# Kernel tuning notes

Hardware: AMD Instinct MI355X
Metric: run time of the kernel (lower is better)

Reference implementation:

```python
import jax, jax.numpy as jnp
import numpy as np

D_MODEL = 2048
HQ = 32          # query heads
HKV = 8          # kv heads
HD = D_MODEL // HQ   # head_dim = 64
G = HQ // HKV        # group size = 4
THETA = 10000.0


def _rope(x, pos):
    """x: (B, H, T, D), pos: (B, T) int. Rotates even/odd interleaved pairs."""
    D = x.shape[-1]
    inv_freq = THETA ** (-jnp.arange(0, D, 2, dtype=jnp.float32) / D)   # (D/2,)
    ang = pos[:, None, :, None].astype(jnp.float32) * inv_freq          # (B,1,T,D/2)
    cos, sin = jnp.cos(ang), jnp.sin(ang)
    x1, x2 = x[..., 0::2], x[..., 1::2]
    r1 = x1 * cos - x2 * sin
    r2 = x1 * sin + x2 * cos
    return jnp.stack([r1, r2], axis=-1).reshape(x.shape)


def setup_inputs() -> dict:
    key = jax.random.key(0)
    ks = jax.random.split(key, 5)
    B, T = 2, 2048
    s = lambda fan_in: 1.0 / np.sqrt(fan_in)
    return {
        "x": jax.random.normal(ks[0], (B, T, D_MODEL), jnp.float32),
        "token_positions": jnp.arange(T, dtype=jnp.int32),
        "WQ": jax.random.normal(ks[1], (HQ * HD, D_MODEL), jnp.float32) * s(D_MODEL),
        "WK": jax.random.normal(ks[2], (HKV * HD, D_MODEL), jnp.float32) * s(D_MODEL),
        "WV": jax.random.normal(ks[3], (HKV * HD, D_MODEL), jnp.float32) * s(D_MODEL),
        "WO": jax.random.normal(ks[4], (D_MODEL, HQ * HD), jnp.float32) * s(HQ * HD),
    }


def reference(x, token_positions, WQ, WK, WV, WO):
    B, T, _ = x.shape
    pos = token_positions if token_positions.ndim == 2 else jnp.broadcast_to(token_positions[None, :], (B, T))

    # Projections (Linear is y = x @ W.T, no bias)
    Q = (x @ WQ.T).reshape(B, T, HQ, HD).transpose(0, 2, 1, 3)    # (B,Hq,T,D)
    K = (x @ WK.T).reshape(B, T, HKV, HD).transpose(0, 2, 1, 3)   # (B,Hkv,T,D)
    V = (x @ WV.T).reshape(B, T, HKV, HD).transpose(0, 2, 1, 3)

    Q = _rope(Q, pos)
    K = _rope(K, pos)

    # GQA: group query heads per kv head instead of duplicating K/V
    Qg = Q.reshape(B, HKV, G, T, HD)
    scale = jnp.float32(1.0 / np.sqrt(HD))
    scores = jnp.einsum('bkgqd,bkld->bkgql', Qg, K) * scale       # (B,Hkv,G,T,T)

    causal = jnp.tril(jnp.ones((T, T), dtype=bool))
    scores = jnp.where(causal, scores, jnp.finfo(scores.dtype).min)
    A = jax.nn.softmax(scores, axis=-1)

    O = jnp.einsum('bkgql,bkld->bkgqd', A, V)                     # (B,Hkv,G,T,D)
    O = O.reshape(B, HQ, T, HD).transpose(0, 2, 1, 3).reshape(B, T, HQ * HD)
    return O @ WO.T
```

## Files before the change

kernel.cpp:

```cpp
#include <hip/hip_runtime.h>
#include <hip/hip_bf16.h>

#define B_   2
#define T_   2048
#define DM_  2048
#define HQ_  32
#define HKV_ 8
#define HD_  64

typedef __attribute__((ext_vector_type(8))) short bf16x8;
typedef __attribute__((ext_vector_type(4))) float f32x4;
typedef __fp16 f16x4 __attribute__((ext_vector_type(4)));
typedef __fp16 f16x2 __attribute__((ext_vector_type(2)));

__device__ __forceinline__ unsigned short f2bf(float f) {
    unsigned int u = __float_as_uint(f);
    u = (u + 0x7fffu + ((u >> 16) & 1u)) >> 16;
    return (unsigned short)u;
}

__device__ __forceinline__ void gload16(const unsigned short* g, unsigned short* l) {
    __builtin_amdgcn_global_load_lds(
        (const __attribute__((address_space(1))) unsigned int*)g,
        (__attribute__((address_space(3))) unsigned int*)l, 16, 0, 0);
}


#define CONV_N 4718592

__global__ __launch_bounds__(256) void convert_all(
    const float* __restrict__ x,  const float* __restrict__ WQ,
    const float* __restrict__ WK, const float* __restrict__ WV,
    const float* __restrict__ WO, unsigned short* __restrict__ ws,
    const int* __restrict__ pos,  float* __restrict__ trig)
{
    int i = blockIdx.x*256 + threadIdx.x;
    if (i >= CONV_N) {
        int j = i - CONV_N;
        if (j < T_*32) {
            int t = j >> 5, p = j & 31;
            float inv = exp2f(-0.4152410118609203f * (float)p);
            float ang = (float)pos[t] * inv;
            float sn, cs;
            sincosf(ang, &sn, &cs);
            *(float2*)&trig[j*2] = make_float2(cs, sn);
        }
        return;
    }
    const float* src; unsigned short* dst; int rel;
    if (i < 2097152)      { src = x;  dst = ws;                 rel = i; }
    else if (i < 3145728) { src = WQ; dst = ws + 8388608;       rel = i - 2097152; }
    else if (i < 3407872) { src = WK; dst = ws + 8388608+4194304; rel = i - 3145728; }
    else if (i < 3670016) { src = WV; dst = ws + 8388608+5242880; rel = i - 3407872; }
    else                  { src = WO; dst = ws + 14680064;      rel = i - 3670016; }
    float4 v = *(const float4*)(src + (size_t)rel*4);
    uint2 pk;
    pk.x = (unsigned int)f2bf(v.x) | ((unsigned int)f2bf(v.y) << 16);
    pk.y = (unsigned int)f2bf(v.z) | ((unsigned int)f2bf(v.w) << 16);
    *(uint2*)(dst + (size_t)rel*4) = pk;
}

__global__ __launch_bounds__(256) void qkv_gemm_bf16(
    const unsigned short* __restrict__ Ab, const unsigned short* __restrict__ Wb,
    unsigned short* __restrict__ Qb, unsigned short* __restrict__ Kb,
    unsigned short* __restrict__ Vt, const float* __restrict__ trig)
{
    __shared__ unsigned short As[3][128*32];
    __shared__ unsigned short Bs[3][128*32];
    const int tid  = threadIdx.x;
    const int ln   = tid & 63;
    const int wv   = tid >> 6;
    const int wm   = (wv >> 1) * 64;
    const int wn   = (wv & 1) * 64;
    const int col  = ln & 15;
    const int quad = ln >> 4;

    const int bid = blockIdx.x;
    const int swz = (bid & 7) * 96 + (bid >> 3);
    const int n0  = (swz % 24) * 128;
    const int m0  = (swz / 24) * 128;

    const int cg = ((tid & 3) ^ ((tid >> 3) & 3)) * 8;
    const unsigned short* aG = Ab + (size_t)(m0 + (tid>>2))*DM_ + cg;
    const unsigned short* bG = Wb + (size_t)(n0 + (tid>>2))*DM_ + cg;
    const int ck = (quad ^ ((col >> 1) & 3)) * 8;

    f32x4 acc[4][4];
    #pragma unroll
    for (int i=0;i<4;++i)
        #pragma unroll
        for (int j=0;j<4;++j) { acc[i][j][0]=0.f; acc[i][j][1]=0.f; acc[i][j][2]=0.f; acc[i][j][3]=0.f; }

    auto stage = [&](int buf, int k0) {
        unsigned short* aL = &As[buf][wv*512];
        unsigned short* bL = &Bs[buf][wv*512];
        gload16(aG + k0,                  aL);
        gload16(aG + (size_t)64*DM_ + k0, aL + 2048);
        gload16(bG + k0,                  bL);
        gload16(bG + (size_t)64*DM_ + k0, bL + 2048);
    };

    auto kstep = [&](int bc, int k0v, int bstage, bool dostage, bool last) {
        if (last) asm volatile("s_waitcnt vmcnt(0)" ::: "memory");
        else      asm volatile("s_waitcnt vmcnt(4)" ::: "memory");
        __builtin_amdgcn_s_barrier();
        if (dostage) stage(bstage, k0v + 64);
        const unsigned short* Ac = As[bc];
        const unsigned short* Bc = Bs[bc];
        bf16x8 af[4], bfr[4];
        #pragma unroll
        for (int i2=0;i2<4;++i2) {
            af[i2]  = *(const bf16x8*)&Ac[(wm + i2*16 + col)*32 + ck];
            bfr[i2] = *(const bf16x8*)&Bc[(wn + i2*16 + col)*32 + ck];
        }
        #pragma unroll
        for (int i2=0;i2<4;++i2)
            #pragma unroll
            for (int j2=0;j2<4;++j2)
                acc[i2][j2] = __builtin_amdgcn_mfma_f32_16x16x32_bf16(af[i2], bfr[j2], acc[i2][j2], 0, 0, 0);
    };

    stage(0, 0);
    stage(1, 32);

    int k0 = 0;
    for (int rep = 0; rep < 20; ++rep) {
        kstep(0, k0,      2, true, false);
        kstep(1, k0+32,   0, true, false);
        kstep(2, k0+64,   1, true, false);
        k0 += 96;
    }
    kstep(0, 1920, 2, true,  false);
    kstep(1, 1952, 0, true,  false);
    kstep(2, 1984, 1, false, false);
    kstep(0, 2016, 0, false, true);

    const int b  = m0 >> 11;
    const int tb = m0 & 2047;
    #pragma unroll
    for (int j=0;j<4;++j) {
        const int n = n0 + wn + j*16 + col;
        if (n < 2560) {
            const int d   = n & 63;
            const int p   = d >> 1;
            const bool ev = (d & 1) == 0;
            const float sc = (n < 2048) ? 0.18033688011112042f : 1.0f;
            unsigned short* outp = (n < 2048)
                ? Qb + (((size_t)(b*HQ_  + (n>>6)))*T_)*HD_
                : Kb + (((size_t)(b*HKV_ + ((n-2048)>>6)))*T_)*HD_;
            #pragma unroll
            for (int i=0;i<4;++i) {
                const int t0 = tb + wm + i*16 + quad*4;
                #pragma unroll
                for (int r=0;r<4;++r) {
                    float self = acc[i][j][r];
                    float part = __shfl_xor(self, 1);
                    float2 cs  = *(const float2*)&trig[((t0 + r)*32 + p)*2];
                    float out  = ev ? (self*cs.x - part*cs.y)
                                    : (part*cs.y + self*cs.x);
                    out *= sc;
                    unsigned int pk = (unsigned int)f2bf(out);
                    unsigned int po = __shfl_xor(pk, 1);
                    if (ev)
                        *(unsigned int*)(outp + (size_t)(t0 + r)*HD_ + d) = pk | (po << 16);
                }
            }
        } else {
            #pragma unroll
            for (int i=0;i<4;++i) {
                const int t = tb + wm + i*16 + quad*4;
                unsigned short* vp = Vt + (((size_t)(b*HKV_ + ((n-2560)>>6)))*HD_ + (n&63))*T_ + t;
                union { f16x2 h; unsigned int u; } c0, c1;
                c0.h = __builtin_amdgcn_cvt_pkrtz(acc[i][j][0], acc[i][j][1]);
                c1.h = __builtin_amdgcn_cvt_pkrtz(acc[i][j][2], acc[i][j][3]);
                *(unsigned int*)(vp)     = c0.u;
                *(unsigned int*)(vp + 2) = c1.u;
            }
        }
    }
}

__global__ __launch_bounds__(256, 2) void attn_mfma(
    const unsigned short* __restrict__ Qb, const unsigned short* __restrict__ Kb,
    const unsigned short* __restrict__ Vh, unsigned short* __restrict__ Ob)
{
    __shared__ unsigned short Ks[2][64*64];
    __shared__ unsigned short Vs[2][64*64];

    const int tid  = threadIdx.x;
    const int lane = tid & 63;
    const int wave = tid >> 6;
    const int q16  = lane & 15;
    const int quad = lane >> 4;
    const int bxi  = blockIdx.x;
    const int bh   = blockIdx.y;
    const int b    = bh >> 5;
    const int h    = bh & 31;
    const int kvh  = h >> 2;
    const int qa   = bxi;
    const int qbt  = 31 - bxi;
    const int qgA  = qa *64 + wave*16 + q16;
    const int qgB  = qbt*64 + wave*16 + q16;

    const unsigned short* kbase = Kb + ((size_t)(b*HKV_ + kvh))*T_*HD_;
    const unsigned short* vbase = Vh + ((size_t)(b*HKV_ + kvh))*(size_t)HD_*T_;

    const bf16x8 qA0 = *(const bf16x8*)(Qb + ((size_t)bh*T_ + qgA)*HD_ + quad*8);
    const bf16x8 qA1 = *(const bf16x8*)(Qb + ((size_t)bh*T_ + qgA)*HD_ + 32 + quad*8);
    const bf16x8 qB0 = *(const bf16x8*)(Qb + ((size_t)bh*T_ + qgB)*HD_ + quad*8);
    const bf16x8 qB1 = *(const bf16x8*)(Qb + ((size_t)bh*T_ + qgB)*HD_ + 32 + quad*8);

    f32x4 oA[4], oB[4];
    #pragma unroll
    for (int i=0;i<4;++i) {
        oA[i][0]=0.f; oA[i][1]=0.f; oA[i][2]=0.f; oA[i][3]=0.f;
        oB[i][0]=0.f; oB[i][1]=0.f; oB[i][2]=0.f; oB[i][3]=0.f;
    }
    float lA = 0.f, lB = 0.f;

    const int sr = tid >> 3;
    const int sj = tid & 7;
    const int sc = (sj ^ (sr & 7)) * 8;

    const int rk7 = q16 & 7;
    const int ck0 = (quad ^ rk7) * 8;
    const int ck1 = ((quad + 4) ^ rk7) * 8;

    auto smrow = [&](const f32x4 s, float& ps) -> f16x4 {
        float e0 = exp2f(s[0]), e1 = exp2f(s[1]);
        float e2 = exp2f(s[2]), e3 = exp2f(s[3]);
        ps += (e0+e1) + (e2+e3);
        union { f16x2 h[2]; f16x4 v; } c;
        c.h[0] = __builtin_amdgcn_cvt_pkrtz(e0, e1);
        c.h[1] = __builtin_amdgcn_cvt_pkrtz(e2, e3);
        return c.v;
    };

    auto tile_barrier = [&]() {
        asm volatile("s_waitcnt lgkmcnt(0)" ::: "memory");
        __builtin_amdgcn_s_barrier();
        __builtin_amdgcn_sched_barrier(0);
    };

    uint4 kr0, kr1, vr0, vr1;
    kr0 = *(const uint4*)(kbase + (size_t)sr*HD_ + sj*8);
    kr1 = *(const uint4*)(kbase + (size_t)(sr+32)*HD_ + sj*8);
    vr0 = *(const uint4*)(vbase + (size_t)sr*T_ + sj*8);
    vr1 = *(const uint4*)(vbase + (size_t)(sr+32)*T_ + sj*8);
    *(uint4*)&Ks[0][sr*64 + sc]      = kr0;
    *(uint4*)&Ks[0][(sr+32)*64 + sc] = kr1;
    *(uint4*)&Vs[0][sr*64 + sc]      = vr0;
    *(uint4*)&Vs[0][(sr+32)*64 + sc] = vr1;
    kr0 = *(const uint4*)(kbase + (size_t)(64+sr)*HD_ + sj*8);
    kr1 = *(const uint4*)(kbase + (size_t)(64+sr+32)*HD_ + sj*8);
    vr0 = *(const uint4*)(vbase + (size_t)sr*T_ + 64 + sj*8);
    vr1 = *(const uint4*)(vbase + (size_t)(sr+32)*T_ + 64 + sj*8);
    __syncthreads();

    int cur = 0;

    for (int kt = 0; kt <= qa; ++kt) {
        const unsigned short* KsC = Ks[cur];
        const unsigned short* VsC = Vs[cur];
        const int nxt = cur ^ 1;

        f32x4 sB[4], sA[4];
        #pragma unroll
        for (int t=0;t<4;++t) {
            sB[t][0]=0.f; sB[t][1]=0.f; sB[t][2]=0.f; sB[t][3]=0.f;
            sA[t][0]=0.f; sA[t][1]=0.f; sA[t][2]=0.f; sA[t][3]=0.f;
        }
        f16x4 pfB[4];
        float psB = 0.f, psA = 0.f;

        __builtin_amdgcn_s_setprio(1);
        #pragma unroll
        for (int t = 0; t < 4; ++t) {
            const int rk = (t*16 + q16) * 64;
            bf16x8 a0 = *(const bf16x8*)&KsC[rk + ck0];
            bf16x8 a1 = *(const bf16x8*)&KsC[rk + ck1];
            sB[t] = __builtin_amdgcn_mfma_f32_16x16x32_bf16(a0, qB0, sB[t], 0, 0, 0);
            sB[t] = __builtin_amdgcn_mfma_f32_16x16x32_bf16(a1, qB1, sB[t], 0, 0, 0);
            sA[t] = __builtin_amdgcn_mfma_f32_16x16x32_bf16(a0, qA0, sA[t], 0, 0, 0);
            sA[t] = __builtin_amdgcn_mfma_f32_16x16x32_bf16(a1, qA1, sA[t], 0, 0, 0);
            if (t > 0) pfB[t-1] = smrow(sB[t-1], psB);
        }
        *(uint4*)&Ks[nxt][sr*64 + sc]      = kr0;
        *(uint4*)&Ks[nxt][(sr+32)*64 + sc] = kr1;
        *(uint4*)&Vs[nxt][sr*64 + sc]      = vr0;
        *(uint4*)&Vs[nxt][(sr+32)*64 + sc] = vr1;
        if (kt + 1 < qbt) {
            const int kn = (kt+2)*64;
            kr0 = *(const uint4*)(kbase + (size_t)(kn+sr)*HD_ + sj*8);
            kr1 = *(const uint4*)(kbase + (size_t)(kn+sr+32)*HD_ + sj*8);
            vr0 = *(const uint4*)(vbase + (size_t)sr*T_ + kn + sj*8);
            vr1 = *(const uint4*)(vbase + (size_t)(sr+32)*T_ + kn + sj*8);
        }
        pfB[3] = smrow(sB[3], psB);
        lB += psB;

        if (kt == qa) {
            #pragma unroll
            for (int t = 0; t < 4; ++t)
                #pragma unroll
                for (int r = 0; r < 4; ++r)
                    if (kt*64 + t*16 + quad*4 + r > qgA) sA[t][r] = -1e30f;
        }

        #pragma unroll
        for (int t = 0; t < 4; ++t) {
            const int cv = ((2*t + (quad>>1)) ^ rk7) * 8 + (quad&1)*4;
            f16x4 va[4];
            #pragma unroll
            for (int dt=0;dt<4;++dt)
                va[dt] = *(const f16x4*)&VsC[(dt*16 + q16)*64 + cv];
            #pragma unroll
            for (int dt=0;dt<4;++dt)
                oB[dt] = __builtin_amdgcn_mfma_f32_16x16x16f16(va[dt], pfB[t], oB[dt], 0, 0, 0);
            f16x4 pfA = smrow(sA[t], psA);
            #pragma unroll
            for (int dt=0;dt<4;++dt)
                oA[dt] = __builtin_amdgcn_mfma_f32_16x16x16f16(va[dt], pfA, oA[dt], 0, 0, 0);
        }
        lA += psA;
        __builtin_amdgcn_s_setprio(0);
        tile_barrier();
        cur ^= 1;
    }

    for (int kt = qa+1; kt <= qbt; ++kt) {
        const unsigned short* KsC = Ks[cur];
        const unsigned short* VsC = Vs[cur];
        const int nxt = cur ^ 1;

        f32x4 sB[4];
        #pragma unroll
        for (int t=0;t<4;++t) { sB[t][0]=0.f; sB[t][1]=0.f; sB[t][2]=0.f; sB[t][3]=0.f; }

        __builtin_amdgcn_s_setprio(1);
        #pragma unroll
        for (int t = 0; t < 4; ++t) {
            const int rk = (t*16 + q16) * 64;
            bf16x8 a0 = *(const bf16x8*)&KsC[rk + ck0];
            bf16x8 a1 = *(const bf16x8*)&KsC[rk + ck1];
            sB[t] = __builtin_amdgcn_mfma_f32_16x16x32_bf16(a0, qB0, sB[t], 0, 0, 0);
            sB[t] = __builtin_amdgcn_mfma_f32_16x16x32_bf16(a1, qB1, sB[t], 0, 0, 0);
        }
        if (kt < qbt) {
            *(uint4*)&Ks[nxt][sr*64 + sc]      = kr0;
            *(uint4*)&Ks[nxt][(sr+32)*64 + sc] = kr1;
            *(uint4*)&Vs[nxt][sr*64 + sc]      = vr0;
            *(uint4*)&Vs[nxt][(sr+32)*64 + sc] = vr1;
        }
        if (kt + 1 < qbt) {
            const int kn = (kt+2)*64;
            kr0 = *(const uint4*)(kbase + (size_t)(kn+sr)*HD_ + sj*8);
            kr1 = *(const uint4*)(kbase + (size_t)(kn+sr+32)*HD_ + sj*8);
            vr0 = *(const uint4*)(vbase + (size_t)sr*T_ + kn + sj*8);
            vr1 = *(const uint4*)(vbase + (size_t)(sr+32)*T_ + kn + sj*8);
        }
        if (kt == qbt) {
            #pragma unroll
            for (int t = 0; t < 4; ++t)
                #pragma unroll
                for (int r = 0; r < 4; ++r)
                    if (kt*64 + t*16 + quad*4 + r > qgB) sB[t][r] = -1e30f;
        }

        float psB = 0.f;
        #pragma unroll
        for (int t = 0; t < 4; ++t) {
            f16x4 pfB = smrow(sB[t], psB);
            const int cv = ((2*t + (quad>>1)) ^ rk7) * 8 + (quad&1)*4;
            #pragma unroll
            for (int dt=0;dt<4;++dt) {
                f16x4 va = *(const f16x4*)&VsC[(dt*16 + q16)*64 + cv];
                oB[dt] = __builtin_amdgcn_mfma_f32_16x16x16f16(va, pfB, oB[dt], 0, 0, 0);
            }
        }
        lB += psB;
        __builtin_amdgcn_s_setprio(0);
        tile_barrier();
        cur ^= 1;
    }

    lA += __shfl_xor(lA, 16); lA += __shfl_xor(lA, 32);
    lB += __shfl_xor(lB, 16); lB += __shfl_xor(lB, 32);
    const float rlA = 1.0f / lA;
    const float rlB = 1.0f / lB;
    unsigned short* opA = Ob + ((size_t)(b*T_ + qgA))*(HQ_*HD_) + h*HD_;
    unsigned short* opB = Ob + ((size_t)(b*T_ + qgB))*(HQ_*HD_) + h*HD_;
    #pragma unroll
    for (int dt = 0; dt < 4; ++dt) {
        uint2 pa, pb;
        pa.x = (unsigned int)f2bf(oA[dt][0]*rlA) | ((unsigned int)f2bf(oA[dt][1]*rlA) << 16);
        pa.y = (unsigned int)f2bf(oA[dt][2]*rlA) | ((unsigned int)f2bf(oA[dt][3]*rlA) << 16);
        pb.x = (unsigned int)f2bf(oB[dt][0]*rlB) | ((unsigned int)f2bf(oB[dt][1]*rlB) << 16);
        pb.y = (unsigned int)f2bf(oB[dt][2]*rlB) | ((unsigned int)f2bf(oB[dt][3]*rlB) << 16);
        *(uint2*)(opA + dt*16 + quad*4) = pa;
        *(uint2*)(opB + dt*16 + quad*4) = pb;
    }
}

__global__ __launch_bounds__(256) void out_gemm_bf16(
    const unsigned short* __restrict__ Ab, const unsigned short* __restrict__ Wb,
    float* __restrict__ C)
{
    __shared__ unsigned short As[3][128*32];
    __shared__ unsigned short Bs[3][128*32];
    const int tid  = threadIdx.x;
    const int ln   = tid & 63;
    const int wv   = tid >> 6;
    const int wm   = (wv >> 1) * 64;
    const int wn   = (wv & 1) * 64;
    const int col  = ln & 15;
    const int quad = ln >> 4;

    const int bid = blockIdx.x;
    const int swz = (bid & 7) * 64 + (bid >> 3);
    const int n0  = (swz & 15) * 128;
    const int m0  = (swz >> 4) * 128;

    const int cg = ((tid & 3) ^ ((tid >> 3) & 3)) * 8;
    const unsigned short* aG = Ab + (size_t)(m0 + (tid>>2))*DM_ + cg;
    const unsigned short* bG = Wb + (size_t)(n0 + (tid>>2))*DM_ + cg;
    const int ck = (quad ^ ((col >> 1) & 3)) * 8;

    f32x4 acc[4][4];
    #pragma unroll
    for (int i=0;i<4;++i)
        #pragma unroll
        for (int j=0;j<4;++j) { acc[i][j][0]=0.f; acc[i][j][1]=0.f; acc[i][j][2]=0.f; acc[i][j][3]=0.f; }

    auto stage = [&](int buf, int k0) {
        unsigned short* aL = &As[buf][wv*512];
        unsigned short* bL = &Bs[buf][wv*512];
        gload16(aG + k0,                  aL);
        gload16(aG + (size_t)64*DM_ + k0, aL + 2048);
        gload16(bG + k0,                  bL);
        gload16(bG + (size_t)64*DM_ + k0, bL + 2048);
    };

    auto kstep = [&](int bc, int k0v, int bstage, bool dostage, bool last) {
        if (last) asm volatile("s_waitcnt vmcnt(0)" ::: "memory");
        else      asm volatile("s_waitcnt vmcnt(4)" ::: "memory");
        __builtin_amdgcn_s_barrier();
        if (dostage) stage(bstage, k0v + 64);
        const unsigned short* Ac = As[bc];
        const unsigned short* Bc = Bs[bc];
        bf16x8 af[4], bfr[4];
        #pragma unroll
        for (int i2=0;i2<4;++i2) {
            af[i2]  = *(const bf16x8*)&Ac[(wm + i2*16 + col)*32 + ck];
            bfr[i2] = *(const bf16x8*)&Bc[(wn + i2*16 + col)*32 + ck];
        }
        #pragma unroll
        for (int i2=0;i2<4;++i2)
            #pragma unroll
            for (int j2=0;j2<4;++j2)
                acc[i2][j2] = __builtin_amdgcn_mfma_f32_16x16x32_bf16(af[i2], bfr[j2], acc[i2][j2], 0, 0, 0);
    };

    stage(0, 0);
    stage(1, 32);

    int k0 = 0;
    for (int rep = 0; rep < 20; ++rep) {
        kstep(0, k0,      2, true, false);
        kstep(1, k0+32,   0, true, false);
        kstep(2, k0+64,   1, true, false);
        k0 += 96;
    }
    kstep(0, 1920, 2, true,  false);
    kstep(1, 1952, 0, true,  false);
    kstep(2, 1984, 1, false, false);
    kstep(0, 2016, 0, false, true);

    #pragma unroll
    for (int i=0;i<4;++i) {
        const int m = m0 + wm + i*16 + quad*4;
        #pragma unroll
        for (int j=0;j<4;++j) {
            const int n = n0 + wn + j*16 + col;
            #pragma unroll
            for (int r=0;r<4;++r)
                C[(size_t)(m + r)*DM_ + n] = acc[i][j][r];
        }
    }
}

extern "C" void kernel_launch(void* const* d_in, const int* in_sizes, int n_in,
                              void* d_out, int out_size, void* d_ws, size_t ws_size,
                              hipStream_t stream) {
    const float* x   = (const float*)d_in[0];
    const int*   pos = (const int*)  d_in[1];
    const float* WQ  = (const float*)d_in[2];
    const float* WK  = (const float*)d_in[3];
    const float* WV  = (const float*)d_in[4];
    const float* WO  = (const float*)d_in[5];
    float* out = (float*)d_out;

    unsigned short* xb  = (unsigned short*)d_ws;
    unsigned short* Wb  = xb  + (size_t)8388608;
    unsigned short* WOb = Wb  + (size_t)6291456;
    unsigned short* Qb  = WOb + (size_t)4194304;
    unsigned short* Kb  = Qb  + (size_t)8388608;
    unsigned short* Vt  = Kb  + (size_t)2097152;
    unsigned short* Ob  = Vt  + (size_t)2097152;
    float* trig = (float*)Ob;

    convert_all<<<18688, 256, 0, stream>>>(x, WQ, WK, WV, WO, (unsigned short*)d_ws, pos, trig);

    qkv_gemm_bf16<<<768, 256, 0, stream>>>(xb, Wb, Qb, Kb, Vt, trig);

    dim3 g3(16, B_*HQ_);
    attn_mfma<<<g3, 256, 0, stream>>>(Qb, Kb, Vt, Ob);

    out_gemm_bf16<<<512, 256, 0, stream>>>(Ob, WOb, out);
}
```

Before: 305.5 us.

## Enlarge QKV GEMM tile to 256x256 with 8 waves per block

The QKV projection GEMM moves from 128x128 tiles with 4 waves to 256x256 tiles with 8 waves (512 threads). Each wave now computes a 128x64 sub-tile, which raises arithmetic intensity per LDS fragment load and reduces global traffic per FLOP. The trade-off is only 192 blocks on a 256-CU device, so some CUs sit idle, plus larger LDS (96KB) and higher register pressure from 32 accumulators per lane.

```diff
diff --git a/kernel.cpp b/kernel.cpp
--- a/kernel.cpp
+++ b/kernel.cpp
@@ -60,44 +60,44 @@
     *(uint2*)(dst + (size_t)rel*4) = pk;
 }
 
-__global__ __launch_bounds__(256) void qkv_gemm_bf16(
+__global__ __launch_bounds__(512, 2) void qkv_gemm_bf16(
     const unsigned short* __restrict__ Ab, const unsigned short* __restrict__ Wb,
     unsigned short* __restrict__ Qb, unsigned short* __restrict__ Kb,
     unsigned short* __restrict__ Vt, const float* __restrict__ trig)
 {
-    __shared__ unsigned short As[3][128*32];
-    __shared__ unsigned short Bs[3][128*32];
+    __shared__ unsigned short As[3][256*32];
+    __shared__ unsigned short Bs[3][256*32];
     const int tid  = threadIdx.x;
-    const int ln   = tid & 63;
+    const int lane = tid & 63;
     const int wv   = tid >> 6;
-    const int wm   = (wv >> 1) * 64;
-    const int wn   = (wv & 1) * 64;
-    const int col  = ln & 15;
-    const int quad = ln >> 4;
+    const int wr   = wv >> 2;
+    const int wc   = wv & 3;
+    const int n16  = lane & 15;
+    const int quad = lane >> 4;
 
     const int bid = blockIdx.x;
-    const int swz = (bid & 7) * 96 + (bid >> 3);
-    const int n0  = (swz % 24) * 128;
-    const int m0  = (swz / 24) * 128;
+    const int swz = (bid & 7) * 24 + (bid >> 3);
+    const int n0  = (swz % 12) * 256;
+    const int m0  = (swz / 12) * 256;
 
     const int cg = ((tid & 3) ^ ((tid >> 3) & 3)) * 8;
     const unsigned short* aG = Ab + (size_t)(m0 + (tid>>2))*DM_ + cg;
     const unsigned short* bG = Wb + (size_t)(n0 + (tid>>2))*DM_ + cg;
-    const int ck = (quad ^ ((col >> 1) & 3)) * 8;
-
-    f32x4 acc[4][4];
+    const int ck = (quad ^ ((n16 >> 1) & 3)) * 8;
+
+    f32x4 acc[8][4];
     #pragma unroll
-    for (int i=0;i<4;++i)
+    for (int i=0;i<8;++i)
         #pragma unroll
         for (int j=0;j<4;++j) { acc[i][j][0]=0.f; acc[i][j][1]=0.f; acc[i][j][2]=0.f; acc[i][j][3]=0.f; }
 
-    auto stage = [&](int buf, int k0) {
+    auto stage = [&](int buf, int k0v) {
         unsigned short* aL = &As[buf][wv*512];
         unsigned short* bL = &Bs[buf][wv*512];
-        gload16(aG + k0,                  aL);
-        gload16(aG + (size_t)64*DM_ + k0, aL + 2048);
-        gload16(bG + k0,                  bL);
-        gload16(bG + (size_t)64*DM_ + k0, bL + 2048);
+        gload16(aG + k0v,                   aL);
+        gload16(aG + (size_t)128*DM_ + k0v, aL + 4096);
+        gload16(bG + k0v,                   bL);
+        gload16(bG + (size_t)128*DM_ + k0v, bL + 4096);
     };
 
     auto kstep = [&](int bc, int k0v, int bstage, bool dostage, bool last) {
@@ -107,14 +107,15 @@
         if (dostage) stage(bstage, k0v + 64);
         const unsigned short* Ac = As[bc];
         const unsigned short* Bc = Bs[bc];
-        bf16x8 af[4], bfr[4];
-        #pragma unroll
-        for (int i2=0;i2<4;++i2) {
-            af[i2]  = *(const bf16x8*)&Ac[(wm + i2*16 + col)*32 + ck];
-            bfr[i2] = *(const bf16x8*)&Bc[(wn + i2*16 + col)*32 + ck];
-        }
-        #pragma unroll
-        for (int i2=0;i2<4;++i2)
+        bf16x8 af[8], bfr[4];
+        #pragma unroll
+        for (int i2=0;i2<8;++i2)
+            af[i2]  = *(const bf16x8*)&Ac[(wr*128 + i2*16 + n16)*32 + ck];
+        #pragma unroll
+        for (int j2=0;j2<4;++j2)
+            bfr[j2] = *(const bf16x8*)&Bc[(wc*64 + j2*16 + n16)*32 + ck];
+        #pragma unroll
+        for (int i2=0;i2<8;++i2)
             #pragma unroll
             for (int j2=0;j2<4;++j2)
                 acc[i2][j2] = __builtin_amdgcn_mfma_f32_16x16x32_bf16(af[i2], bfr[j2], acc[i2][j2], 0, 0, 0);
@@ -137,25 +138,26 @@
 
     const int b  = m0 >> 11;
     const int tb = m0 & 2047;
+    const float2* trig2 = (const float2*)trig;
     #pragma unroll
-    for (int j=0;j<4;++j) {
-        const int n = n0 + wn + j*16 + col;
+    for (int nf=0; nf<4; ++nf) {
+        const int n = n0 + wc*64 + nf*16 + n16;
         if (n < 2560) {
             const int d   = n & 63;
             const int p   = d >> 1;
             const bool ev = (d & 1) == 0;
             const float sc = (n < 2048) ? 0.18033688011112042f : 1.0f;
             unsigned short* outp = (n < 2048)
-                ? Qb + (((size_t)(b*HQ_  + (n>>6)))*T_)*HD_
-                : Kb + (((size_t)(b*HKV_ + ((n-2048)>>6)))*T_)*HD_;
-            #pragma unroll
-            for (int i=0;i<4;++i) {
-                const int t0 = tb + wm + i*16 + quad*4;
+                ? Qb + ((size_t)(b*HQ_  + (n>>6)))*T_*HD_
+                : Kb + ((size_t)(b*HKV_ + ((n-2048)>>6)))*T_*HD_;
+            #pragma unroll
+            for (int mf=0; mf<8; ++mf) {
+                const int t0 = tb + wr*128 + mf*16 + quad*4;
                 #pragma unroll
                 for (int r=0;r<4;++r) {
-                    float self = acc[i][j][r];
+                    float self = acc[mf][nf][r];
                     float part = __shfl_xor(self, 1);
-                    float2 cs  = *(const float2*)&trig[((t0 + r)*32 + p)*2];
+                    float2 cs  = trig2[(t0 + r)*32 + p];
                     float out  = ev ? (self*cs.x - part*cs.y)
                                     : (part*cs.y + self*cs.x);
                     out *= sc;
@@ -166,13 +168,15 @@
                 }
             }
         } else {
-            #pragma unroll
-            for (int i=0;i<4;++i) {
-                const int t = tb + wm + i*16 + quad*4;
-                unsigned short* vp = Vt + (((size_t)(b*HKV_ + ((n-2560)>>6)))*HD_ + (n&63))*T_ + t;
+            const int d  = n & 63;
+            const int vh = (n - 2560) >> 6;
+            #pragma unroll
+            for (int mf=0; mf<8; ++mf) {
+                const int t = tb + wr*128 + mf*16 + quad*4;
+                unsigned short* vp = Vt + ((size_t)(b*HKV_ + vh)*HD_ + d)*T_ + t;
                 union { f16x2 h; unsigned int u; } c0, c1;
-                c0.h = __builtin_amdgcn_cvt_pkrtz(acc[i][j][0], acc[i][j][1]);
-                c1.h = __builtin_amdgcn_cvt_pkrtz(acc[i][j][2], acc[i][j][3]);
+                c0.h = __builtin_amdgcn_cvt_pkrtz(acc[mf][nf][0], acc[mf][nf][1]);
+                c1.h = __builtin_amdgcn_cvt_pkrtz(acc[mf][nf][2], acc[mf][nf][3]);
                 *(unsigned int*)(vp)     = c0.u;
                 *(unsigned int*)(vp + 2) = c1.u;
             }
@@ -511,7 +515,7 @@
 
     convert_all<<<18688, 256, 0, stream>>>(x, WQ, WK, WV, WO, (unsigned short*)d_ws, pos, trig);
 
-    qkv_gemm_bf16<<<768, 256, 0, stream>>>(xb, Wb, Qb, Kb, Vt, trig);
+    qkv_gemm_bf16<<<192, 512, 0, stream>>>(xb, Wb, Qb, Kb, Vt, trig);
 
     dim3 g3(16, B_*HQ_);
     attn_mfma<<<g3, 256, 0, stream>>>(Qb, Kb, Vt, Ob);
```

New measurement: 321.1 us. 5.1% more time.

## Split paired query tiles across separate waves in 512-thread attention blocks

Applied to the files above, without the earlier changes.

The attention kernel now launches 512 threads per block. Waves 0-3 handle the long (late) query tile and waves 4-7 handle the short (early) tile, where before each wave processed both tiles. Each wave holds one set of Q, O and score registers, which lowers register pressure and lets more waves be resident. The cost is that the short-tile waves sit idle at barriers while the long tile finishes, since every wave still walks the full K/V loop to help with shared-memory loads.

```diff
diff --git a/kernel.cpp b/kernel.cpp
--- a/kernel.cpp
+++ b/kernel.cpp
@@ -180,7 +180,7 @@
     }
 }
 
-__global__ __launch_bounds__(256, 2) void attn_mfma(
+__global__ __launch_bounds__(512, 4) void attn_mfma(
     const unsigned short* __restrict__ Qb, const unsigned short* __restrict__ Kb,
     const unsigned short* __restrict__ Vh, unsigned short* __restrict__ Ob)
 {
@@ -189,7 +189,7 @@
 
     const int tid  = threadIdx.x;
     const int lane = tid & 63;
-    const int wave = tid >> 6;
+    const int wv   = tid >> 6;
     const int q16  = lane & 15;
     const int quad = lane >> 4;
     const int bxi  = blockIdx.x;
@@ -199,24 +199,20 @@
     const int kvh  = h >> 2;
     const int qa   = bxi;
     const int qbt  = 31 - bxi;
-    const int qgA  = qa *64 + wave*16 + q16;
-    const int qgB  = qbt*64 + wave*16 + q16;
+    const bool isB = (wv < 4);
+    const int  kact = isB ? qbt : qa;
+    const int  myq  = (isB ? qbt*64 + wv*16 : qa*64 + (wv-4)*16) + q16;
 
     const unsigned short* kbase = Kb + ((size_t)(b*HKV_ + kvh))*T_*HD_;
     const unsigned short* vbase = Vh + ((size_t)(b*HKV_ + kvh))*(size_t)HD_*T_;
 
-    const bf16x8 qA0 = *(const bf16x8*)(Qb + ((size_t)bh*T_ + qgA)*HD_ + quad*8);
-    const bf16x8 qA1 = *(const bf16x8*)(Qb + ((size_t)bh*T_ + qgA)*HD_ + 32 + quad*8);
-    const bf16x8 qB0 = *(const bf16x8*)(Qb + ((size_t)bh*T_ + qgB)*HD_ + quad*8);
-    const bf16x8 qB1 = *(const bf16x8*)(Qb + ((size_t)bh*T_ + qgB)*HD_ + 32 + quad*8);
-
-    f32x4 oA[4], oB[4];
-    #pragma unroll
-    for (int i=0;i<4;++i) {
-        oA[i][0]=0.f; oA[i][1]=0.f; oA[i][2]=0.f; oA[i][3]=0.f;
-        oB[i][0]=0.f; oB[i][1]=0.f; oB[i][2]=0.f; oB[i][3]=0.f;
-    }
-    float lA = 0.f, lB = 0.f;
+    const bf16x8 q0 = *(const bf16x8*)(Qb + ((size_t)bh*T_ + myq)*HD_ + quad*8);
+    const bf16x8 q1 = *(const bf16x8*)(Qb + ((size_t)bh*T_ + myq)*HD_ + 32 + quad*8);
+
+    f32x4 o[4];
+    #pragma unroll
+    for (int i=0;i<4;++i) { o[i][0]=0.f; o[i][1]=0.f; o[i][2]=0.f; o[i][3]=0.f; }
+    float l = 0.f;
 
     const int sr = tid >> 3;
     const int sj = tid & 7;
@@ -230,9 +226,9 @@
         float e0 = exp2f(s[0]), e1 = exp2f(s[1]);
         float e2 = exp2f(s[2]), e3 = exp2f(s[3]);
         ps += (e0+e1) + (e2+e3);
-        union { f16x2 h[2]; f16x4 v; } c;
-        c.h[0] = __builtin_amdgcn_cvt_pkrtz(e0, e1);
-        c.h[1] = __builtin_amdgcn_cvt_pkrtz(e2, e3);
+        union { f16x2 hh[2]; f16x4 v; } c;
+        c.hh[0] = __builtin_amdgcn_cvt_pkrtz(e0, e1);
+        c.hh[1] = __builtin_amdgcn_cvt_pkrtz(e2, e3);
         return c.v;
     };
 
@@ -242,163 +238,79 @@
         __builtin_amdgcn_sched_barrier(0);
     };
 
-    uint4 kr0, kr1, vr0, vr1;
-    kr0 = *(const uint4*)(kbase + (size_t)sr*HD_ + sj*8);
-    kr1 = *(const uint4*)(kbase + (size_t)(sr+32)*HD_ + sj*8);
-    vr0 = *(const uint4*)(vbase + (size_t)sr*T_ + sj*8);
-    vr1 = *(const uint4*)(vbase + (size_t)(sr+32)*T_ + sj*8);
-    *(uint4*)&Ks[0][sr*64 + sc]      = kr0;
-    *(uint4*)&Ks[0][(sr+32)*64 + sc] = kr1;
-    *(uint4*)&Vs[0][sr*64 + sc]      = vr0;
-    *(uint4*)&Vs[0][(sr+32)*64 + sc] = vr1;
-    kr0 = *(const uint4*)(kbase + (size_t)(64+sr)*HD_ + sj*8);
-    kr1 = *(const uint4*)(kbase + (size_t)(64+sr+32)*HD_ + sj*8);
-    vr0 = *(const uint4*)(vbase + (size_t)sr*T_ + 64 + sj*8);
-    vr1 = *(const uint4*)(vbase + (size_t)(sr+32)*T_ + 64 + sj*8);
+    uint4 kr, vr;
+    kr = *(const uint4*)(kbase + (size_t)sr*HD_ + sj*8);
+    vr = *(const uint4*)(vbase + (size_t)sr*T_ + sj*8);
+    *(uint4*)&Ks[0][sr*64 + sc] = kr;
+    *(uint4*)&Vs[0][sr*64 + sc] = vr;
+    kr = *(const uint4*)(kbase + (size_t)(64+sr)*HD_ + sj*8);
+    vr = *(const uint4*)(vbase + (size_t)sr*T_ + 64 + sj*8);
     __syncthreads();
 
     int cur = 0;
-
-    for (int kt = 0; kt <= qa; ++kt) {
-        const unsigned short* KsC = Ks[cur];
-        const unsigned short* VsC = Vs[cur];
+    for (int kt = 0; kt <= qbt; ++kt) {
         const int nxt = cur ^ 1;
-
-        f32x4 sB[4], sA[4];
-        #pragma unroll
-        for (int t=0;t<4;++t) {
-            sB[t][0]=0.f; sB[t][1]=0.f; sB[t][2]=0.f; sB[t][3]=0.f;
-            sA[t][0]=0.f; sA[t][1]=0.f; sA[t][2]=0.f; sA[t][3]=0.f;
-        }
-        f16x4 pfB[4];
-        float psB = 0.f, psA = 0.f;
-
-        __builtin_amdgcn_s_setprio(1);
-        #pragma unroll
-        for (int t = 0; t < 4; ++t) {
-            const int rk = (t*16 + q16) * 64;
-            bf16x8 a0 = *(const bf16x8*)&KsC[rk + ck0];
-            bf16x8 a1 = *(const bf16x8*)&KsC[rk + ck1];
-            sB[t] = __builtin_amdgcn_mfma_f32_16x16x32_bf16(a0, qB0, sB[t], 0, 0, 0);
-            sB[t] = __builtin_amdgcn_mfma_f32_16x16x32_bf16(a1, qB1, sB[t], 0, 0, 0);
-            sA[t] = __builtin_amdgcn_mfma_f32_16x16x32_bf16(a0, qA0, sA[t], 0, 0, 0);
-            sA[t] = __builtin_amdgcn_mfma_f32_16x16x32_bf16(a1, qA1, sA[t], 0, 0, 0);
-            if (t > 0) pfB[t-1] = smrow(sB[t-1], psB);
-        }
-        *(uint4*)&Ks[nxt][sr*64 + sc]      = kr0;
-        *(uint4*)&Ks[nxt][(sr+32)*64 + sc] = kr1;
-        *(uint4*)&Vs[nxt][sr*64 + sc]      = vr0;
-        *(uint4*)&Vs[nxt][(sr+32)*64 + sc] = vr1;
+        if (kt <= kact) {
+            const unsigned short* KsC = Ks[cur];
+            const unsigned short* VsC = Vs[cur];
+            f32x4 s[4];
+            #pragma unroll
+            for (int t=0;t<4;++t) { s[t][0]=0.f; s[t][1]=0.f; s[t][2]=0.f; s[t][3]=0.f; }
+
+            __builtin_amdgcn_s_setprio(1);
+            #pragma unroll
+            for (int t = 0; t < 4; ++t) {
+                const int rk = (t*16 + q16) * 64;
+                bf16x8 a0 = *(const bf16x8*)&KsC[rk + ck0];
+                bf16x8 a1 = *(const bf16x8*)&KsC[rk + ck1];
+                s[t] = __builtin_amdgcn_mfma_f32_16x16x32_bf16(a0, q0, s[t], 0, 0, 0);
+                s[t] = __builtin_amdgcn_mfma_f32_16x16x32_bf16(a1, q1, s[t], 0, 0, 0);
+            }
+            if (kt == kact) {
+                #pragma unroll
+                for (int t = 0; t < 4; ++t)
+                    #pragma unroll
+                    for (int r = 0; r < 4; ++r)
+                        if (kt*64 + t*16 + quad*4 + r > myq) s[t][r] = -1e30f;
+            }
+            f16x4 pf[4];
+            float ps = 0.f;
+            #pragma unroll
+            for (int t = 0; t < 4; ++t) pf[t] = smrow(s[t], ps);
+            #pragma unroll
+            for (int t = 0; t < 4; ++t) {
+                const int cv = ((2*t + (quad>>1)) ^ rk7) * 8 + (quad&1)*4;
+                #pragma unroll
+                for (int dt=0;dt<4;++dt) {
+                    f16x4 va = *(const f16x4*)&VsC[(dt*16 + q16)*64 + cv];
+                    o[dt] = __builtin_amdgcn_mfma_f32_16x16x16f16(va, pf[t], o[dt], 0, 0, 0);
+                }
+            }
+            __builtin_amdgcn_s_setprio(0);
+            l += ps;
+        }
+        if (kt < qbt) {
+            *(uint4*)&Ks[nxt][sr*64 + sc] = kr;
+            *(uint4*)&Vs[nxt][sr*64 + sc] = vr;
+        }
         if (kt + 1 < qbt) {
             const int kn = (kt+2)*64;
-            kr0 = *(const uint4*)(kbase + (size_t)(kn+sr)*HD_ + sj*8);
-            kr1 = *(const uint4*)(kbase + (size_t)(kn+sr+32)*HD_ + sj*8);
-            vr0 = *(const uint4*)(vbase + (size_t)sr*T_ + kn + sj*8);
-            vr1 = *(const uint4*)(vbase + (size_t)(sr+32)*T_ + kn + sj*8);
-        }
-        pfB[3] = smrow(sB[3], psB);
-        lB += psB;
-
-        if (kt == qa) {
-            #pragma unroll
-            for (int t = 0; t < 4; ++t)
-                #pragma unroll
-                for (int r = 0; r < 4; ++r)
-                    if (kt*64 + t*16 + quad*4 + r > qgA) sA[t][r] = -1e30f;
-        }
-
-        #pragma unroll
-        for (int t = 0; t < 4; ++t) {
-            const int cv = ((2*t + (quad>>1)) ^ rk7) * 8 + (quad&1)*4;
-            f16x4 va[4];
-            #pragma unroll
-            for (int dt=0;dt<4;++dt)
-                va[dt] = *(const f16x4*)&VsC[(dt*16 + q16)*64 + cv];
-            #pragma unroll
-            for (int dt=0;dt<4;++dt)
-                oB[dt] = __builtin_amdgcn_mfma_f32_16x16x16f16(va[dt], pfB[t], oB[dt], 0, 0, 0);
-            f16x4 pfA = smrow(sA[t], psA);
-            #pragma unroll
-            for (int dt=0;dt<4;++dt)
-                oA[dt] = __builtin_amdgcn_mfma_f32_16x16x16f16(va[dt], pfA, oA[dt], 0, 0, 0);
-        }
-        lA += psA;
-        __builtin_amdgcn_s_setprio(0);
+            kr = *(const uint4*)(kbase + (size_t)(kn+sr)*HD_ + sj*8);
+            vr = *(const uint4*)(vbase + (size_t)sr*T_ + kn + sj*8);
+        }
         tile_barrier();
         cur ^= 1;
     }
 
-    for (int kt = qa+1; kt <= qbt; ++kt) {
-        const unsigned short* KsC = Ks[cur];
-        const unsigned short* VsC = Vs[cur];
-        const int nxt = cur ^ 1;
-
-        f32x4 sB[4];
-        #pragma unroll
-        for (int t=0;t<4;++t) { sB[t][0]=0.f; sB[t][1]=0.f; sB[t][2]=0.f; sB[t][3]=0.f; }
-
-        __builtin_amdgcn_s_setprio(1);
-        #pragma unroll
-        for (int t = 0; t < 4; ++t) {
-            const int rk = (t*16 + q16) * 64;
-            bf16x8 a0 = *(const bf16x8*)&KsC[rk + ck0];
-            bf16x8 a1 = *(const bf16x8*)&KsC[rk + ck1];
-            sB[t] = __builtin_amdgcn_mfma_f32_16x16x32_bf16(a0, qB0, sB[t], 0, 0, 0);
-            sB[t] = __builtin_amdgcn_mfma_f32_16x16x32_bf16(a1, qB1, sB[t], 0, 0, 0);
-        }
-        if (kt < qbt) {
-            *(uint4*)&Ks[nxt][sr*64 + sc]      = kr0;
-            *(uint4*)&Ks[nxt][(sr+32)*64 + sc] = kr1;
-            *(uint4*)&Vs[nxt][sr*64 + sc]      = vr0;
-            *(uint4*)&Vs[nxt][(sr+32)*64 + sc] = vr1;
-        }
-        if (kt + 1 < qbt) {
-            const int kn = (kt+2)*64;
-            kr0 = *(const uint4*)(kbase + (size_t)(kn+sr)*HD_ + sj*8);
-            kr1 = *(const uint4*)(kbase + (size_t)(kn+sr+32)*HD_ + sj*8);
-            vr0 = *(const uint4*)(vbase + (size_t)sr*T_ + kn + sj*8);
-            vr1 = *(const uint4*)(vbase + (size_t)(sr+32)*T_ + kn + sj*8);
-        }
-        if (kt == qbt) {
-            #pragma unroll
-            for (int t = 0; t < 4; ++t)
-                #pragma unroll
-                for (int r = 0; r < 4; ++r)
-                    if (kt*64 + t*16 + quad*4 + r > qgB) sB[t][r] = -1e30f;
-        }
-
-        float psB = 0.f;
-        #pragma unroll
-        for (int t = 0; t < 4; ++t) {
-            f16x4 pfB = smrow(sB[t], psB);
-            const int cv = ((2*t + (quad>>1)) ^ rk7) * 8 + (quad&1)*4;
-            #pragma unroll
-            for (int dt=0;dt<4;++dt) {
-                f16x4 va = *(const f16x4*)&VsC[(dt*16 + q16)*64 + cv];
-                oB[dt] = __builtin_amdgcn_mfma_f32_16x16x16f16(va, pfB, oB[dt], 0, 0, 0);
-            }
-        }
-        lB += psB;
-        __builtin_amdgcn_s_setprio(0);
-        tile_barrier();
-        cur ^= 1;
-    }
-
-    lA += __shfl_xor(lA, 16); lA += __shfl_xor(lA, 32);
-    lB += __shfl_xor(lB, 16); lB += __shfl_xor(lB, 32);
-    const float rlA = 1.0f / lA;
-    const float rlB = 1.0f / lB;
-    unsigned short* opA = Ob + ((size_t)(b*T_ + qgA))*(HQ_*HD_) + h*HD_;
-    unsigned short* opB = Ob + ((size_t)(b*T_ + qgB))*(HQ_*HD_) + h*HD_;
+    l += __shfl_xor(l, 16); l += __shfl_xor(l, 32);
+    const float rl = 1.0f / l;
+    unsigned short* op = Ob + ((size_t)(b*T_ + myq))*(HQ_*HD_) + h*HD_;
     #pragma unroll
     for (int dt = 0; dt < 4; ++dt) {
-        uint2 pa, pb;
-        pa.x = (unsigned int)f2bf(oA[dt][0]*rlA) | ((unsigned int)f2bf(oA[dt][1]*rlA) << 16);
-        pa.y = (unsigned int)f2bf(oA[dt][2]*rlA) | ((unsigned int)f2bf(oA[dt][3]*rlA) << 16);
-        pb.x = (unsigned int)f2bf(oB[dt][0]*rlB) | ((unsigned int)f2bf(oB[dt][1]*rlB) << 16);
-        pb.y = (unsigned int)f2bf(oB[dt][2]*rlB) | ((unsigned int)f2bf(oB[dt][3]*rlB) << 16);
-        *(uint2*)(opA + dt*16 + quad*4) = pa;
-        *(uint2*)(opB + dt*16 + quad*4) = pb;
+        uint2 pk;
+        pk.x = (unsigned int)f2bf(o[dt][0]*rl) | ((unsigned int)f2bf(o[dt][1]*rl) << 16);
+        pk.y = (unsigned int)f2bf(o[dt][2]*rl) | ((unsigned int)f2bf(o[dt][3]*rl) << 16);
+        *(uint2*)(op + dt*16 + quad*4) = pk;
     }
 }
 
@@ -514,7 +426,7 @@
     qkv_gemm_bf16<<<768, 256, 0, stream>>>(xb, Wb, Qb, Kb, Vt, trig);
 
     dim3 g3(16, B_*HQ_);
-    attn_mfma<<<g3, 256, 0, stream>>>(Qb, Kb, Vt, Ob);
+    attn_mfma<<<g3, 512, 0, stream>>>(Qb, Kb, Vt, Ob);
 
     out_gemm_bf16<<<512, 256, 0, stream>>>(Ob, WOb, out);
 }
```

New measurement: 311.8 us. 2.1% more time.
